# Kernel tuning notes

Hardware: AMD Instinct MI355X
Metric: run time of the kernel (lower is better)

Reference implementation:

```python
import jax, jax.numpy as jnp
import numpy as np

B, T, S, E, H = 4, 32, 256, 512, 8
D = E // H
SCALE = np.sqrt(D).astype(np.float32)
Q_MOD, K_MOD = 0, 1


def setup_inputs() -> dict:
    key = jax.random.key(0)
    ks = jax.random.split(key, 12)
    def spikes(k):
        return (jax.random.uniform(k, (B, T, S, E)) < 0.1).astype(jnp.float32)
    init = lambda k, shp: jax.random.normal(k, shp, dtype=jnp.float32) * (1.0 / np.sqrt(shp[0]))
    return {
        "query_spikes": spikes(ks[0]),
        "key_spikes": spikes(ks[1]),
        "value_spikes": spikes(ks[2]),
        "Wq": init(ks[3], (E, E)), "bq": jnp.zeros((E,), jnp.float32),
        "Wk": init(ks[4], (E, E)), "bk": jnp.zeros((E,), jnp.float32),
        "Wv": init(ks[5], (E, E)), "bv": jnp.zeros((E,), jnp.float32),
        "Wo": init(ks[6], (E, E)), "bo": jnp.zeros((E,), jnp.float32),
        "modality_weights": jnp.ones((2, H), jnp.float32),          # nn.Parameter(torch.ones(2, num_heads))
        "temporal_sync": jax.random.normal(ks[7], (T, H), jnp.float32) * 0.1,  # torch.randn(T, H) * 0.1
    }


def _spike_softmax(scores):
    # sigmoid((s - max)*5) normalized along key axis
    m = jnp.max(scores, axis=-1, keepdims=True)
    p = jax.nn.sigmoid((scores - m) * 5.0)
    return p / (jnp.sum(p, axis=-1, keepdims=True) + 1e-8)


def reference(query_spikes, key_spikes, value_spikes, Wq, bq, Wk, bk, Wv, bv, Wo, bo,
              modality_weights, temporal_sync):
    def proj(x, W, b):  # [B,T,S,E] -> [B,T,H,S,D]
        y = jnp.einsum("btse,ef->btsf", x, W) + b
        return y.reshape(B, T, S, H, D).transpose(0, 1, 3, 2, 4)

    Q = proj(query_spikes, Wq, bq)
    K = proj(key_spikes, Wk, bk)
    V = proj(value_spikes, Wv, bv)

    # attention scores across all timesteps at once: [B,T,H,Sq,Sk]
    scores = jnp.einsum("bthqd,bthkd->bthqk", Q, K) / SCALE
    mod_w = (modality_weights[Q_MOD] * modality_weights[K_MOD]).reshape(1, 1, H, 1, 1)
    scores = scores * mod_w + temporal_sync.reshape(1, T, H, 1, 1)

    attn = _spike_softmax(scores)
    attended = jnp.einsum("bthqk,bthkd->bthqd", attn, V)   # [B,T,H,Sq,D]
    attended = attended.transpose(0, 1, 3, 2, 4).reshape(B, T, S, E)
    return jnp.einsum("btse,ef->btsf", attended, Wo) + bo
```

## Files before the change

### kernel.cpp

```cpp
#include <hip/hip_runtime.h>
#include <hip/hip_bf16.h>

#define DI __device__ __forceinline__

typedef __bf16 bf16x8 __attribute__((ext_vector_type(8)));
typedef float  f32x4  __attribute__((ext_vector_type(4)));
typedef float  f32x16 __attribute__((ext_vector_type(16)));
typedef unsigned u32x4 __attribute__((ext_vector_type(4)));


DI ushort f2bf(float f) {
  union { float f; unsigned u; } v; v.f = f;
  unsigned r = v.u + 0x7fffu + ((v.u >> 16) & 1u);
  return (ushort)(r >> 16);
}

DI unsigned cvtpk2(float a, float b) {
  unsigned r;
  asm("v_cvt_pk_bf16_f32 %0, %1, %2" : "=v"(r) : "v"(a), "v"(b));
  return r;
}

DI float rcpf(float x) {
  float r;
  asm("v_rcp_f32 %0, %1" : "=v"(r) : "v"(x));
  return r;
}

DI void gload_lds16(const void* g, void* lds) {
  __builtin_amdgcn_global_load_lds(
      (const __attribute__((address_space(1))) unsigned*)g,
      (__attribute__((address_space(3))) unsigned*)lds, 16, 0, 0);
}

#define WAITVM8   asm volatile("s_waitcnt vmcnt(8)" ::: "memory")
#define WAITVM4   asm volatile("s_waitcnt vmcnt(4)" ::: "memory")
#define WAITVM0   asm volatile("s_waitcnt vmcnt(0)" ::: "memory")
#define WAITLGKM0 asm volatile("s_waitcnt lgkmcnt(0)" ::: "memory")
#define SBAR      __builtin_amdgcn_s_barrier()

DI f32x4 zero4() { f32x4 z; z[0] = 0.f; z[1] = 0.f; z[2] = 0.f; z[3] = 0.f; return z; }

DI f32x16 zero16() {
  f32x16 z;
  for (int i = 0; i < 16; i++) z[i] = 0.f;
  return z;
}

union BF8U { ushort u[8]; unsigned d[4]; bf16x8 v; };

__global__ __launch_bounds__(256) void prep_kernel(
    const float* __restrict__ W0, const float* __restrict__ W1,
    const float* __restrict__ W2, const float* __restrict__ W3,
    ushort* __restrict__ wt,
    const float* __restrict__ q, const float* __restrict__ k,
    const float* __restrict__ v, unsigned* __restrict__ bits) {
  __shared__ unsigned char Nib[16][128];
  int bid = blockIdx.x, tid = threadIdx.x, z = blockIdx.y;
  const float* src = (z == 0 ? q : z == 1 ? k : v) + (size_t)bid * 8192;

  unsigned char nibs[8];
#pragma unroll
  for (int i = 0; i < 8; i++) {
    int c = i * 256 + tid;
    u32x4 a = *(const u32x4*)(src + c * 4);
    nibs[i] = (unsigned char)((a[0] != 0u) | ((a[1] != 0u) << 1) |
                              ((a[2] != 0u) << 2) | ((a[3] != 0u) << 3));
  }
#pragma unroll
  for (int i = 0; i < 8; i++) {
    int c = i * 256 + tid;
    Nib[c >> 7][c & 127] = nibs[i];
  }
  __syncthreads();

  int r = tid >> 4, q16 = tid & 15;
  unsigned out = 0;
#pragma unroll
  for (int b = 0; b < 4; b++) {
    int j = q16 * 4 + b;
    int sub = j >> 3, t = j & 7;
    unsigned lo = Nib[r][t * 16 + sub * 2];
    unsigned hi = Nib[r][t * 16 + sub * 2 + 1];
    out |= (lo | (hi << 4)) << (8 * b);
  }
  bits[(size_t)z * 524288 + bid * 256 + tid] = out;

  if (z == 0 && bid < 256) {
    __shared__ float tile[64][65];
    int wsel = bid >> 6, tl = bid & 63;
    const float* W = wsel == 0 ? W0 : wsel == 1 ? W1 : wsel == 2 ? W2 : W3;
    ushort* o = wt + (size_t)wsel * 512 * 512;
    int k0 = (tl >> 3) * 64, n0 = (tl & 7) * 64;
#pragma unroll
    for (int i = 0; i < 16; i++) {
      int idx = i * 256 + tid; int rr = idx >> 6, c = idx & 63;
      tile[rr][c] = W[(size_t)(k0 + rr) * 512 + n0 + c];
    }
    __syncthreads();
#pragma unroll
    for (int i = 0; i < 16; i++) {
      int idx = i * 256 + tid; int rr = idx >> 6, c = idx & 63;
      o[(size_t)(n0 + rr) * 512 + k0 + c] = f2bf(tile[c][rr]);
    }
  }
}

__global__ __launch_bounds__(256, 4) void qkv_gemm_kernel(
    const unsigned char* __restrict__ Abits, const ushort* __restrict__ Wt,
    const float* __restrict__ bqp, const float* __restrict__ bkp,
    const float* __restrict__ bvp,
    ushort* __restrict__ Qw, ushort* __restrict__ Kw, ushort* __restrict__ Vt) {
  __shared__ __align__(16) char Blds[32768];
  __shared__ __align__(16) char Lut[128];
  int z = blockIdx.z;
  const unsigned char* Ab8 = Abits + (size_t)z * 2097152;
  const ushort* Bt = Wt + (size_t)z * 262144;
  const float* bias = z == 0 ? bqp : z == 1 ? bkp : bvp;
  int bl = ((int)blockIdx.x & 7) * 128 + ((int)blockIdx.x >> 3);
  int m0 = (bl >> 2) * 128, n0 = (bl & 3) * 128;
  int tid = threadIdx.x, lane = tid & 63, wv = tid >> 6;
  int wm = (wv >> 1) * 64, wn = (wv & 1) * 64;
  int hi4 = lane >> 4;

  if (tid < 16) {
    unsigned n = (unsigned)tid;
    uint2 e;
    e.x = (n & 1u ? 0x3F80u : 0u) | (n & 2u ? 0x3F800000u : 0u);
    e.y = (n & 4u ? 0x3F80u : 0u) | (n & 8u ? 0x3F800000u : 0u);
    *(uint2*)(&Lut[n * 8]) = e;
  }

  f32x4 acc[4][4];
#pragma unroll
  for (int i = 0; i < 4; i++)
#pragma unroll
    for (int j = 0; j < 4; j++) acc[i][j] = zero4();

  uint2 abits[4][2];
#pragma unroll
  for (int i = 0; i < 4; i++)
#pragma unroll
    for (int ks = 0; ks < 2; ks++)
      abits[i][ks] = *(const uint2*)(Ab8 + (size_t)(m0 + wm + i * 16 + (lane & 15)) * 64
                                     + (ks * 4 + hi4) * 8);

  auto expandA = [&](int i, int ks, int t) -> bf16x8 {
    unsigned w = t < 4 ? abits[i][ks].x >> (8 * t) : abits[i][ks].y >> (8 * (t - 4));
    unsigned wb = w & 255u;
    uint2 lo = *(const uint2*)(&Lut[(wb & 15u) * 8]);
    uint2 hi = *(const uint2*)(&Lut[(wb >> 4) * 8]);
    BF8U av;
    av.d[0] = lo.x; av.d[1] = lo.y; av.d[2] = hi.x; av.d[3] = hi.y;
    return av.v;
  };
  auto issueB = [&](int t) {
    char* Bb = Blds + (t & 1) * 16384;
#pragma unroll
    for (int i = 0; i < 4; i++) {
      int c = (wv * 4 + i) * 64 + lane;
      int r = c >> 3, g = (c & 7) ^ (r & 7);
      gload_lds16(Bt + (size_t)(n0 + r) * 512 + t * 64 + g * 8, Bb + (wv * 4 + i) * 1024);
    }
  };
  auto compute = [&](int t) {
    char* Bb = Blds + (t & 1) * 16384;
#pragma unroll
    for (int ks = 0; ks < 2; ks++) {
      bf16x8 a[4], b[4];
#pragma unroll
      for (int i = 0; i < 4; i++) {
        int rb = wn + i * 16 + (lane & 15);
        b[i] = *(const bf16x8*)(Bb + ((rb * 128 + (ks * 4 + hi4) * 16) ^ ((rb & 7) << 4)));
        a[i] = expandA(i, ks, t);
      }
#pragma unroll
      for (int i = 0; i < 4; i++)
#pragma unroll
        for (int j = 0; j < 4; j++)
          acc[i][j] = __builtin_amdgcn_mfma_f32_16x16x32_bf16(a[i], b[j], acc[i][j], 0, 0, 0);
    }
  };

  WAITLGKM0;
  issueB(0); issueB(1);
#pragma unroll
  for (int t = 0; t < 8; t++) {
    if (t < 7) { WAITVM4; } else { WAITVM0; }
    SBAR;
    compute(t);
    WAITLGKM0;
    SBAR;
    if (t < 6) issueB(t + 2);
  }

#pragma unroll
  for (int j = 0; j < 4; j++) {
    int col = n0 + wn + j * 16 + (lane & 15);
    float bv = bias[col];
#pragma unroll
    for (int i = 0; i < 4; i++) {
      int row0 = m0 + wm + i * 16 + (lane >> 4) * 4;
      if (z == 2) {
        int btv = row0 >> 8, s = row0 & 255;
        ushort4 w;
        w.x = f2bf(acc[i][j][0] + bv); w.y = f2bf(acc[i][j][1] + bv);
        w.z = f2bf(acc[i][j][2] + bv); w.w = f2bf(acc[i][j][3] + bv);
        *(ushort4*)(Vt + ((size_t)btv * 512 + col) * 256 + s) = w;
      } else {
        ushort* C = z == 0 ? Qw : Kw;
#pragma unroll
        for (int r = 0; r < 4; r++)
          C[(size_t)(row0 + r) * 512 + col] = f2bf(acc[i][j][r] + bv);
      }
    }
  }
}

__global__ __launch_bounds__(256, 2) void out_gemm_kernel(
    const ushort* __restrict__ A, const ushort* __restrict__ Bt,
    const float* __restrict__ bias, float* __restrict__ C) {
  __shared__ __align__(16) char Alds[32768];
  __shared__ __align__(16) char Blds[32768];
  int bl = ((int)blockIdx.x & 7) * 128 + ((int)blockIdx.x >> 3);
  int m0 = (bl >> 2) * 128, n0 = (bl & 3) * 128;
  int tid = threadIdx.x, lane = tid & 63, wv = tid >> 6;
  int wm = (wv >> 1) * 64, wn = (wv & 1) * 64;

  f32x4 acc[4][4];
#pragma unroll
  for (int i = 0; i < 4; i++)
#pragma unroll
    for (int j = 0; j < 4; j++) acc[i][j] = zero4();

  auto stage = [&](int t) {
    char* Ab = Alds + (t & 1) * 16384;
    char* Bb = Blds + (t & 1) * 16384;
#pragma unroll
    for (int i = 0; i < 4; i++) {
      int c = (wv * 4 + i) * 64 + lane;
      int r = c >> 3, g = (c & 7) ^ (r & 7);
      gload_lds16(A + (size_t)(m0 + r) * 512 + t * 64 + g * 8, Ab + (wv * 4 + i) * 1024);
      gload_lds16(Bt + (size_t)(n0 + r) * 512 + t * 64 + g * 8, Bb + (wv * 4 + i) * 1024);
    }
  };
  auto compute = [&](int t) {
    char* Ab = Alds + (t & 1) * 16384;
    char* Bb = Blds + (t & 1) * 16384;
#pragma unroll
    for (int ks = 0; ks < 2; ks++) {
      bf16x8 a[4], b[4];
#pragma unroll
      for (int i = 0; i < 4; i++) {
        int ra = wm + i * 16 + (lane & 15);
        a[i] = *(const bf16x8*)(Ab + ((ra * 128 + (ks * 4 + (lane >> 4)) * 16) ^ ((ra & 7) << 4)));
        int rb = wn + i * 16 + (lane & 15);
        b[i] = *(const bf16x8*)(Bb + ((rb * 128 + (ks * 4 + (lane >> 4)) * 16) ^ ((rb & 7) << 4)));
      }
#pragma unroll
      for (int i = 0; i < 4; i++)
#pragma unroll
        for (int j = 0; j < 4; j++)
          acc[i][j] = __builtin_amdgcn_mfma_f32_16x16x32_bf16(a[i], b[j], acc[i][j], 0, 0, 0);
    }
  };

  stage(0);
  stage(1);
#pragma unroll
  for (int t = 0; t < 8; t++) {
    if (t < 7) { WAITVM8; } else { WAITVM0; }
    SBAR;
    compute(t);
    WAITLGKM0;
    SBAR;
    if (t < 6) stage(t + 2);
  }

  int lane2 = threadIdx.x & 63;
#pragma unroll
  for (int j = 0; j < 4; j++) {
    int col = n0 + wn + j * 16 + (lane2 & 15);
    float bv = bias[col];
#pragma unroll
    for (int i = 0; i < 4; i++) {
      int row0 = m0 + wm + i * 16 + (lane2 >> 4) * 4;
#pragma unroll
      for (int r = 0; r < 4; r++)
        C[(size_t)(row0 + r) * 512 + col] = acc[i][j][r] + bv;
    }
  }
}

__global__ __launch_bounds__(256) void attn_kernel(
    const ushort* __restrict__ Q, const ushort* __restrict__ K,
    const ushort* __restrict__ Vt, const float* __restrict__ mw,
    ushort* __restrict__ att) {
  __shared__ __align__(16) char Klds[32768];
  __shared__ __align__(16) char Vlds[32768];
  int tid = threadIdx.x, lane = tid & 63, wv = tid >> 6;
  int lq = lane & 31, hi = lane >> 5;
  int b = blockIdx.x;
  int h = b & 7, bt = b >> 3;
  const ushort* Qb = Q + ((size_t)bt * 256 + wv * 64) * 512 + h * 64;
  const ushort* Kb = K + ((size_t)bt * 256) * 512 + h * 64;
  const ushort* Vb = Vt + ((size_t)bt * 512 + h * 64) * 256;
  float c0 = mw[h] * mw[8 + h] * 0.125f;

#pragma unroll
  for (int i = 0; i < 8; i++) {
    int ci = (wv * 8 + i) * 64 + lane;
    int l2 = ci & 31, h2 = (ci >> 5) & 1, ds = (ci >> 6) & 3, kt = ci >> 8;
    gload_lds16(Kb + (size_t)(kt * 32 + l2) * 512 + ds * 16 + h2 * 8,
                &Klds[(wv * 8 + i) * 1024]);
  }
  bf16x8 qf[2][4];
#pragma unroll
  for (int qj = 0; qj < 2; qj++)
#pragma unroll
    for (int ds = 0; ds < 4; ds++)
      qf[qj][ds] = *(const bf16x8*)(Qb + (size_t)(qj * 32 + lq) * 512 + ds * 16 + hi * 8);
  __syncthreads();

#pragma unroll
  for (int i = 0; i < 8; i++) {
    int ci = (wv * 8 + i) * 64 + lane;
    int l2 = ci & 31, h2 = (ci >> 5) & 1, df = (ci >> 6) & 1, ks = (ci >> 7) & 1, kt = ci >> 8;
    gload_lds16(Vb + (size_t)(df * 32 + l2) * 256 + kt * 32 + ks * 16 + h2 * 8,
                &Vlds[(wv * 8 + i) * 1024]);
  }

  float mx[2] = {-3.0e38f, -3.0e38f};
#pragma unroll 2
  for (int kt = 0; kt < 8; kt++) {
    bf16x8 kf[4];
#pragma unroll
    for (int ds = 0; ds < 4; ds++)
      kf[ds] = *(const bf16x8*)(&Klds[((kt * 4 + ds) * 2 + hi) * 512 + lq * 16]);
#pragma unroll
    for (int qj = 0; qj < 2; qj++) {
      f32x16 sT = zero16();
#pragma unroll
      for (int ds = 0; ds < 4; ds++)
        sT = __builtin_amdgcn_mfma_f32_32x32x16_bf16(kf[ds], qf[qj][ds], sT, 0, 0, 0);
#pragma unroll
      for (int r = 0; r < 16; r++) mx[qj] = fmaxf(mx[qj], sT[r] * c0);
    }
  }
#pragma unroll
  for (int qj = 0; qj < 2; qj++) mx[qj] = fmaxf(mx[qj], __shfl_xor(mx[qj], 32, 64));
  __syncthreads();

  float a5 = 5.f * c0;
  float m5[2] = {5.f * mx[0], 5.f * mx[1]};
  float sm[2] = {0.f, 0.f};
  f32x16 acc[2][2];
  acc[0][0] = zero16(); acc[0][1] = zero16(); acc[1][0] = zero16(); acc[1][1] = zero16();

#pragma unroll 2
  for (int kt = 0; kt < 8; kt++) {
    bf16x8 kf[4], vf[2][2];
#pragma unroll
    for (int ds = 0; ds < 4; ds++)
      kf[ds] = *(const bf16x8*)(&Klds[((kt * 4 + ds) * 2 + hi) * 512 + lq * 16]);
#pragma unroll
    for (int ks = 0; ks < 2; ks++)
#pragma unroll
      for (int df = 0; df < 2; df++)
        vf[ks][df] = *(const bf16x8*)(&Vlds[(((kt * 2 + ks) * 2 + df) * 2 + hi) * 512 + lq * 16]);
#pragma unroll
    for (int qj = 0; qj < 2; qj++) {
      f32x16 sT = zero16();
#pragma unroll
      for (int ds = 0; ds < 4; ds++)
        sT = __builtin_amdgcn_mfma_f32_32x32x16_bf16(kf[ds], qf[qj][ds], sT, 0, 0, 0);
      unsigned pk[8];
#pragma unroll
      for (int i = 0; i < 8; i++) {
        float p0 = rcpf(1.f + __expf(m5[qj] - sT[2 * i] * a5));
        float p1 = rcpf(1.f + __expf(m5[qj] - sT[2 * i + 1] * a5));
        sm[qj] += p0 + p1;
        pk[i] = cvtpk2(p0, p1);
      }
#pragma unroll
      for (int ks = 0; ks < 2; ks++) {
        int bb = ks * 4;
        unsigned sa = (unsigned)__shfl_xor((int)pk[bb + 0], 32, 64);
        unsigned sb = (unsigned)__shfl_xor((int)pk[bb + 1], 32, 64);
        unsigned sc = (unsigned)__shfl_xor((int)pk[bb + 2], 32, 64);
        unsigned sd = (unsigned)__shfl_xor((int)pk[bb + 3], 32, 64);
        BF8U pa;
        pa.d[0] = hi ? sc : pk[bb + 0];
        pa.d[1] = hi ? sd : pk[bb + 1];
        pa.d[2] = hi ? pk[bb + 2] : sa;
        pa.d[3] = hi ? pk[bb + 3] : sb;
#pragma unroll
        for (int df = 0; df < 2; df++)
          acc[qj][df] = __builtin_amdgcn_mfma_f32_32x32x16_bf16(pa.v, vf[ks][df], acc[qj][df], 0, 0, 0);
      }
    }
  }

#pragma unroll
  for (int qj = 0; qj < 2; qj++) sm[qj] += __shfl_xor(sm[qj], 32, 64);
  float rs[2] = {rcpf(sm[0] + 1e-8f), rcpf(sm[1] + 1e-8f)};
#pragma unroll
  for (int qj = 0; qj < 2; qj++) {
#pragma unroll
    for (int r = 0; r < 16; r++) {
      int ql = (r & 3) + 8 * (r >> 2) + 4 * hi;
      float rr = __shfl(rs[qj], ql, 64);
      size_t rowbase = ((size_t)bt * 256 + wv * 64 + qj * 32 + ql) * 512 + h * 64;
#pragma unroll
      for (int df = 0; df < 2; df++)
        att[rowbase + df * 32 + lq] = f2bf(acc[qj][df][r] * rr);
    }
  }
}

extern "C" void kernel_launch(void* const* d_in, const int* in_sizes, int n_in,
                              void* d_out, int out_size, void* d_ws, size_t ws_size,
                              hipStream_t stream) {
  (void)in_sizes; (void)n_in; (void)out_size; (void)ws_size;
  const float* qs  = (const float*)d_in[0];
  const float* ksn = (const float*)d_in[1];
  const float* vsn = (const float*)d_in[2];
  const float* Wq  = (const float*)d_in[3];
  const float* bq  = (const float*)d_in[4];
  const float* Wk  = (const float*)d_in[5];
  const float* bk  = (const float*)d_in[6];
  const float* Wv  = (const float*)d_in[7];
  const float* bv  = (const float*)d_in[8];
  const float* Wo  = (const float*)d_in[9];
  const float* bo  = (const float*)d_in[10];
  const float* mw  = (const float*)d_in[11];

  char* ws = (char*)d_ws;
  const size_t SLOT = 33554432u;
  ushort* Wt = (ushort*)ws;
  unsigned char* Abits = (unsigned char*)(ws + (size_t)(2u << 20));
  char*   s0 = ws + (size_t)(8u << 20);
  ushort* Qw = (ushort*)(s0 + 0 * SLOT);
  ushort* Kw = (ushort*)(s0 + 1 * SLOT);
  ushort* Vt = (ushort*)(s0 + 2 * SLOT);
  ushort* Aw = (ushort*)(s0 + 3 * SLOT);

  prep_kernel<<<dim3(2048, 3), 256, 0, stream>>>(Wq, Wk, Wv, Wo, Wt, qs, ksn, vsn,
                                                 (unsigned*)Abits);
  qkv_gemm_kernel<<<dim3(1024, 1, 3), 256, 0, stream>>>(Abits, Wt, bq, bk, bv,
                                                        Qw, Kw, Vt);
  attn_kernel<<<dim3(1024), 256, 0, stream>>>(Qw, Kw, Vt, mw, Aw);
  out_gemm_kernel<<<dim3(1024), 256, 0, stream>>>(Aw, Wt + 3 * 262144, bo, (float*)d_out);
}
```

Before: 183.8 us.

## Fuse spike bit-packing into QKV GEMM and loop over all N tiles per block

Result: slower. 293.7 us (+59.8%).

```diff
diff --git a/kernel.cpp b/kernel.cpp
--- a/kernel.cpp
+++ b/kernel.cpp
@@ -49,76 +49,43 @@
 
 union BF8U { ushort u[8]; unsigned d[4]; bf16x8 v; };
 
-__global__ __launch_bounds__(256) void prep_kernel(
+__global__ __launch_bounds__(256) void wtrans_kernel(
     const float* __restrict__ W0, const float* __restrict__ W1,
     const float* __restrict__ W2, const float* __restrict__ W3,
-    ushort* __restrict__ wt,
+    ushort* __restrict__ out) {
+  __shared__ float tile[64][65];
+  const float* W = blockIdx.z == 0 ? W0 : blockIdx.z == 1 ? W1 : blockIdx.z == 2 ? W2 : W3;
+  ushort* o = out + (size_t)blockIdx.z * 512 * 512;
+  int k0 = blockIdx.x * 64, n0 = blockIdx.y * 64;
+  int tid = threadIdx.x;
+#pragma unroll
+  for (int i = 0; i < 16; i++) {
+    int idx = i * 256 + tid; int r = idx >> 6, c = idx & 63;
+    tile[r][c] = W[(size_t)(k0 + r) * 512 + n0 + c];
+  }
+  __syncthreads();
+#pragma unroll
+  for (int i = 0; i < 16; i++) {
+    int idx = i * 256 + tid; int r = idx >> 6, c = idx & 63;
+    o[(size_t)(n0 + r) * 512 + k0 + c] = f2bf(tile[c][r]);
+  }
+}
+
+__global__ __launch_bounds__(256, 3) void qkv_gemm_kernel(
     const float* __restrict__ q, const float* __restrict__ k,
-    const float* __restrict__ v, unsigned* __restrict__ bits) {
-  __shared__ unsigned char Nib[16][128];
-  int bid = blockIdx.x, tid = threadIdx.x, z = blockIdx.y;
-  const float* src = (z == 0 ? q : z == 1 ? k : v) + (size_t)bid * 8192;
-
-  unsigned char nibs[8];
-#pragma unroll
-  for (int i = 0; i < 8; i++) {
-    int c = i * 256 + tid;
-    u32x4 a = *(const u32x4*)(src + c * 4);
-    nibs[i] = (unsigned char)((a[0] != 0u) | ((a[1] != 0u) << 1) |
-                              ((a[2] != 0u) << 2) | ((a[3] != 0u) << 3));
-  }
-#pragma unroll
-  for (int i = 0; i < 8; i++) {
-    int c = i * 256 + tid;
-    Nib[c >> 7][c & 127] = nibs[i];
-  }
-  __syncthreads();
-
-  int r = tid >> 4, q16 = tid & 15;
-  unsigned out = 0;
-#pragma unroll
-  for (int b = 0; b < 4; b++) {
-    int j = q16 * 4 + b;
-    int sub = j >> 3, t = j & 7;
-    unsigned lo = Nib[r][t * 16 + sub * 2];
-    unsigned hi = Nib[r][t * 16 + sub * 2 + 1];
-    out |= (lo | (hi << 4)) << (8 * b);
-  }
-  bits[(size_t)z * 524288 + bid * 256 + tid] = out;
-
-  if (z == 0 && bid < 256) {
-    __shared__ float tile[64][65];
-    int wsel = bid >> 6, tl = bid & 63;
-    const float* W = wsel == 0 ? W0 : wsel == 1 ? W1 : wsel == 2 ? W2 : W3;
-    ushort* o = wt + (size_t)wsel * 512 * 512;
-    int k0 = (tl >> 3) * 64, n0 = (tl & 7) * 64;
-#pragma unroll
-    for (int i = 0; i < 16; i++) {
-      int idx = i * 256 + tid; int rr = idx >> 6, c = idx & 63;
-      tile[rr][c] = W[(size_t)(k0 + rr) * 512 + n0 + c];
-    }
-    __syncthreads();
-#pragma unroll
-    for (int i = 0; i < 16; i++) {
-      int idx = i * 256 + tid; int rr = idx >> 6, c = idx & 63;
-      o[(size_t)(n0 + rr) * 512 + k0 + c] = f2bf(tile[c][rr]);
-    }
-  }
-}
-
-__global__ __launch_bounds__(256, 4) void qkv_gemm_kernel(
-    const unsigned char* __restrict__ Abits, const ushort* __restrict__ Wt,
+    const float* __restrict__ v, const ushort* __restrict__ Wt,
     const float* __restrict__ bqp, const float* __restrict__ bkp,
     const float* __restrict__ bvp,
     ushort* __restrict__ Qw, ushort* __restrict__ Kw, ushort* __restrict__ Vt) {
   __shared__ __align__(16) char Blds[32768];
+  __shared__ __align__(16) char Bits[8192];
+  __shared__ unsigned char Nib[16][128];
   __shared__ __align__(16) char Lut[128];
-  int z = blockIdx.z;
-  const unsigned char* Ab8 = Abits + (size_t)z * 2097152;
+  int z = blockIdx.y;
+  const float* Af = (z == 0 ? q : z == 1 ? k : v) + (size_t)blockIdx.x * 65536;
   const ushort* Bt = Wt + (size_t)z * 262144;
   const float* bias = z == 0 ? bqp : z == 1 ? bkp : bvp;
-  int bl = ((int)blockIdx.x & 7) * 128 + ((int)blockIdx.x >> 3);
-  int m0 = (bl >> 2) * 128, n0 = (bl & 3) * 128;
+  int m0 = blockIdx.x * 128;
   int tid = threadIdx.x, lane = tid & 63, wv = tid >> 6;
   int wm = (wv >> 1) * 64, wn = (wv & 1) * 64;
   int hi4 = lane >> 4;
@@ -131,18 +98,40 @@
     *(uint2*)(&Lut[n * 8]) = e;
   }
 
-  f32x4 acc[4][4];
+  int pr = tid >> 4, q16 = tid & 15;
+  for (int g = 0; g < 8; g++) {
+    unsigned char nibs[8];
+#pragma unroll
+    for (int i = 0; i < 8; i++) {
+      int c = i * 256 + tid;
+      u32x4 a = *(const u32x4*)(Af + (size_t)g * 8192 + c * 4);
+      nibs[i] = (unsigned char)((a[0] != 0u) | ((a[1] != 0u) << 1) |
+                                ((a[2] != 0u) << 2) | ((a[3] != 0u) << 3));
+    }
+#pragma unroll
+    for (int i = 0; i < 8; i++) {
+      int c = i * 256 + tid;
+      Nib[c >> 7][c & 127] = nibs[i];
+    }
+    __syncthreads();
+    unsigned out = 0;
+#pragma unroll
+    for (int b = 0; b < 4; b++) {
+      int j = q16 * 4 + b;
+      int sub = j >> 3, t = j & 7;
+      out |= ((unsigned)Nib[pr][t * 16 + sub * 2] |
+              ((unsigned)Nib[pr][t * 16 + sub * 2 + 1] << 4)) << (8 * b);
+    }
+    ((unsigned*)Bits)[(g * 16 + pr) * 16 + q16] = out;
+    __syncthreads();
+  }
+
+  uint2 abits[4][2];
 #pragma unroll
   for (int i = 0; i < 4; i++)
 #pragma unroll
-    for (int j = 0; j < 4; j++) acc[i][j] = zero4();
-
-  uint2 abits[4][2];
-#pragma unroll
-  for (int i = 0; i < 4; i++)
-#pragma unroll
     for (int ks = 0; ks < 2; ks++)
-      abits[i][ks] = *(const uint2*)(Ab8 + (size_t)(m0 + wm + i * 16 + (lane & 15)) * 64
+      abits[i][ks] = *(const uint2*)(Bits + (wm + i * 16 + (lane & 15)) * 64
                                      + (ks * 4 + hi4) * 8);
 
   auto expandA = [&](int i, int ks, int t) -> bf16x8 {
@@ -154,6 +143,8 @@
     av.d[0] = lo.x; av.d[1] = lo.y; av.d[2] = hi.x; av.d[3] = hi.y;
     return av.v;
   };
+
+  int n0 = 0;
   auto issueB = [&](int t) {
     char* Bb = Blds + (t & 1) * 16384;
 #pragma unroll
@@ -163,55 +154,62 @@
       gload_lds16(Bt + (size_t)(n0 + r) * 512 + t * 64 + g * 8, Bb + (wv * 4 + i) * 1024);
     }
   };
-  auto compute = [&](int t) {
-    char* Bb = Blds + (t & 1) * 16384;
-#pragma unroll
-    for (int ks = 0; ks < 2; ks++) {
-      bf16x8 a[4], b[4];
+
+  f32x4 acc[4][4];
+  for (int nt = 0; nt < 4; nt++) {
+    n0 = nt * 128;
+#pragma unroll
+    for (int i = 0; i < 4; i++)
+#pragma unroll
+      for (int j = 0; j < 4; j++) acc[i][j] = zero4();
+
+    issueB(0); issueB(1);
+#pragma unroll
+    for (int t = 0; t < 8; t++) {
+      if (t < 7) { WAITVM4; } else { WAITVM0; }
+      SBAR;
+      {
+        char* Bb = Blds + (t & 1) * 16384;
+#pragma unroll
+        for (int ks = 0; ks < 2; ks++) {
+          bf16x8 a[4], b[4];
+#pragma unroll
+          for (int i = 0; i < 4; i++) {
+            int rb = wn + i * 16 + (lane & 15);
+            b[i] = *(const bf16x8*)(Bb + ((rb * 128 + (ks * 4 + hi4) * 16) ^ ((rb & 7) << 4)));
+            a[i] = expandA(i, ks, t);
+          }
+#pragma unroll
+          for (int i = 0; i < 4; i++)
+#pragma unroll
+            for (int j = 0; j < 4; j++)
+              acc[i][j] = __builtin_amdgcn_mfma_f32_16x16x32_bf16(a[i], b[j], acc[i][j], 0, 0, 0);
+        }
+      }
+      WAITLGKM0;
+      SBAR;
+      if (t < 6) issueB(t + 2);
+    }
+
+#pragma unroll
+    for (int j = 0; j < 4; j++) {
+      int col = n0 + wn + j * 16 + (lane & 15);
+      float bv = bias[col];
 #pragma unroll
       for (int i = 0; i < 4; i++) {
-        int rb = wn + i * 16 + (lane & 15);
-        b[i] = *(const bf16x8*)(Bb + ((rb * 128 + (ks * 4 + hi4) * 16) ^ ((rb & 7) << 4)));
-        a[i] = expandA(i, ks, t);
-      }
-#pragma unroll
-      for (int i = 0; i < 4; i++)
-#pragma unroll
-        for (int j = 0; j < 4; j++)
-          acc[i][j] = __builtin_amdgcn_mfma_f32_16x16x32_bf16(a[i], b[j], acc[i][j], 0, 0, 0);
-    }
-  };
-
-  WAITLGKM0;
-  issueB(0); issueB(1);
-#pragma unroll
-  for (int t = 0; t < 8; t++) {
-    if (t < 7) { WAITVM4; } else { WAITVM0; }
-    SBAR;
-    compute(t);
-    WAITLGKM0;
-    SBAR;
-    if (t < 6) issueB(t + 2);
-  }
-
-#pragma unroll
-  for (int j = 0; j < 4; j++) {
-    int col = n0 + wn + j * 16 + (lane & 15);
-    float bv = bias[col];
-#pragma unroll
-    for (int i = 0; i < 4; i++) {
-      int row0 = m0 + wm + i * 16 + (lane >> 4) * 4;
-      if (z == 2) {
-        int btv = row0 >> 8, s = row0 & 255;
-        ushort4 w;
-        w.x = f2bf(acc[i][j][0] + bv); w.y = f2bf(acc[i][j][1] + bv);
-        w.z = f2bf(acc[i][j][2] + bv); w.w = f2bf(acc[i][j][3] + bv);
-        *(ushort4*)(Vt + ((size_t)btv * 512 + col) * 256 + s) = w;
-      } else {
-        ushort* C = z == 0 ? Qw : Kw;
-#pragma unroll
-        for (int r = 0; r < 4; r++)
-          C[(size_t)(row0 + r) * 512 + col] = f2bf(acc[i][j][r] + bv);
+        int row0 = m0 + wm + i * 16 + (lane >> 4) * 4;
+        if (z == 2) {
+          int btv = row0 >> 8, s = row0 & 255;
+          ushort4 w;
+          w.x = f2bf(acc[i][j][0] + bv); w.y = f2bf(acc[i][j][1] + bv);
+          w.z = f2bf(acc[i][j][2] + bv); w.w = f2bf(acc[i][j][3] + bv);
+          *(ushort4*)(Vt + ((size_t)btv * 512 + col) * 256 + s) = w;
+        } else {
+          ushort* C = z == 0 ? Qw : Kw;
+#pragma unroll
+          for (int r = 0; r < 4; r++)
+            C[(size_t)(row0 + r) * 512 + col] = f2bf(acc[i][j][r] + bv);
+        }
       }
     }
   }
@@ -438,17 +436,15 @@
   char* ws = (char*)d_ws;
   const size_t SLOT = 33554432u;
   ushort* Wt = (ushort*)ws;
-  unsigned char* Abits = (unsigned char*)(ws + (size_t)(2u << 20));
   char*   s0 = ws + (size_t)(8u << 20);
   ushort* Qw = (ushort*)(s0 + 0 * SLOT);
   ushort* Kw = (ushort*)(s0 + 1 * SLOT);
   ushort* Vt = (ushort*)(s0 + 2 * SLOT);
   ushort* Aw = (ushort*)(s0 + 3 * SLOT);
 
-  prep_kernel<<<dim3(2048, 3), 256, 0, stream>>>(Wq, Wk, Wv, Wo, Wt, qs, ksn, vsn,
-                                                 (unsigned*)Abits);
-  qkv_gemm_kernel<<<dim3(1024, 1, 3), 256, 0, stream>>>(Abits, Wt, bq, bk, bv,
-                                                        Qw, Kw, Vt);
+  wtrans_kernel<<<dim3(8, 8, 4), 256, 0, stream>>>(Wq, Wk, Wv, Wo, Wt);
+  qkv_gemm_kernel<<<dim3(256, 3), 256, 0, stream>>>(qs, ksn, vsn, Wt, bq, bk, bv,
+                                                    Qw, Kw, Vt);
   attn_kernel<<<dim3(1024), 256, 0, stream>>>(Qw, Kw, Vt, mw, Aw);
   out_gemm_kernel<<<dim3(1024), 256, 0, stream>>>(Aw, Wt + 3 * 262144, bo, (float*)d_out);
 }
```
